# Optimization experiments

Hardware: AMD Instinct MI355X
Metric: run time of the kernel (lower is better)

## Reference

```python
import jax, jax.numpy as jnp
import numpy as np

L, N, D, C = 4, 16384, 512, 1000

def setup_inputs() -> dict:
    key = jax.random.key(0)
    k1, k2, k3, k4, k5 = jax.random.split(key, 5)
    feature = jax.random.normal(k1, (L, N, D), dtype=jnp.float32)
    mean = jax.random.normal(k2, (L, C, D), dtype=jnp.float32)
    inverse_cov = jax.random.normal(k3, (L, D, D), dtype=jnp.float32)
    weight = jax.random.uniform(k4, (L,), dtype=jnp.float32)
    top2_index = jax.random.randint(k5, (N,), 0, C, dtype=jnp.int64)
    return {"feature": feature, "mean": mean, "inverse_cov": inverse_cov,
            "weight": weight, "top2_index": top2_index}

def reference(feature, mean, inverse_cov, weight, top2_index):
    # Gather class means per sample: [L, N, D]
    final_mean = mean[:, top2_index, :]
    zero_f = feature - final_mean  # [L, N, D]
    # Diagonal of zero_f @ inv_cov @ zero_f^T without forming the NxN matrix:
    # q[l, n] = sum_{d,e} zero_f[l,n,d] * inv_cov[l,d,e] * zero_f[l,n,e]
    q = jnp.einsum('lnd,lde,lne->ln', zero_f, inverse_cov, zero_f)  # [L, N]
    return jnp.sum(weight * jnp.mean(q, axis=1))
```

## Files before the change

### kernel.cpp

```cpp
#include <hip/hip_runtime.h>
#include <hip/hip_bf16.h>
#include <stdint.h>

#define LDIM 4
#define NDIM 16384
#define DDIM 512
#define CDIM 1000
#define NSTEP 16

#define SYT_ELEMS ((size_t)LDIM * DDIM * DDIM)
#define GH_OFF   (SYT_ELEMS * 2)
#define GH_ELEMS ((size_t)LDIM * CDIM * DDIM)
#define SS_OFF   (GH_OFF + GH_ELEMS * 2)
#define SS_FLOATS ((size_t)LDIM * 1024)
#define WS_NEED  (SS_OFF + SS_FLOATS * 4)

typedef __attribute__((ext_vector_type(8))) _Float16 f16x8;
typedef __attribute__((ext_vector_type(4))) float f32x4;

__device__ __forceinline__ unsigned short f2h(float x) {
  union { _Float16 h; unsigned short u; } c; c.h = (_Float16)x; return c.u;
}
__device__ __forceinline__ float h2f(unsigned short u) {
  union { unsigned short u; _Float16 h; } c; c.u = u; return (float)c.h;
}
__device__ __forceinline__ f16x8 cvt8(float4 a, float4 b) {
  f16x8 p;
  p[0] = (_Float16)a.x; p[1] = (_Float16)a.y; p[2] = (_Float16)a.z; p[3] = (_Float16)a.w;
  p[4] = (_Float16)b.x; p[5] = (_Float16)b.y; p[6] = (_Float16)b.z; p[7] = (_Float16)b.w;
  return p;
}
__device__ __forceinline__ void gload16(const void* g, void* l) {
  __builtin_amdgcn_global_load_lds(
      (const __attribute__((address_space(1))) void*)g,
      (__attribute__((address_space(3))) void*)l, 16, 0, 0);
}

__device__ __forceinline__ size_t syt_off(int l, int d, int k) {
  return ((size_t)(l * NSTEP + (k >> 5)) * DDIM + d) * 32 +
         ((((k & 31) >> 3) + ((d >> 1) & 3)) & 3) * 8 + (k & 7);
}

#define BB0 0
#define AB0 65536
#define IDS_OFF 73728
#define SVAL_OFF 73984
#define RED_OFF 74240
#define LDS_MAIN 74272
#define LDS_PREP 65536

extern "C" __global__ void mel_mconv(const float* __restrict__ IC,
                                     unsigned short* __restrict__ SYT) {
  size_t i4 = (size_t)blockIdx.x * 256 + threadIdx.x;
  size_t base = i4 * 4;
  int l = (int)(base >> 18);
  int rem = (int)(base & 262143);
  int d = rem >> 9;
  int e = rem & 511;
  float4 v = *(const float4*)(IC + base);
  const float* icl = IC + ((size_t)l << 18);
  float t0 = icl[(size_t)(e + 0) * DDIM + d];
  float t1 = icl[(size_t)(e + 1) * DDIM + d];
  float t2 = icl[(size_t)(e + 2) * DDIM + d];
  float t3 = icl[(size_t)(e + 3) * DDIM + d];
  *(ushort4*)(SYT + syt_off(l, d, e)) =
      make_ushort4(f2h(0.5f * (v.x + t0)), f2h(0.5f * (v.y + t1)),
                   f2h(0.5f * (v.z + t2)), f2h(0.5f * (v.w + t3)));
}

extern "C" __global__ __launch_bounds__(512, 2)
void mel_prep(const float* __restrict__ MEAN, const unsigned short* __restrict__ SYT,
              unsigned short* __restrict__ GH, float* __restrict__ SS) {
  extern __shared__ __align__(16) char lds[];
  const int t = threadIdx.x, lane = t & 63, w = t >> 6;
  const int l = blockIdx.x & 3, ct = blockIdx.x >> 2;
  const int row0 = ct * 64;
  const int col0 = w * 64, lrow = lane & 15, lkg = lane >> 4;
  const int lke = lkg << 3;

  {
    const int srow = t >> 3;
    const int grow = row0 + srow;
    const float* mr = MEAN + ((size_t)l * CDIM + grow) * DDIM + ((t & 7) << 3);
    const int swb = srow * 1024 + (((t & 7) ^ (srow & 7)) << 4);
    const float4 z4 = {0.f, 0.f, 0.f, 0.f};
    for (int c = 0; c < 8; ++c) {
      float4 x = z4, y = z4;
      if (grow < CDIM) { x = *(const float4*)(mr + c * 64); y = *(const float4*)(mr + c * 64 + 4); }
      *(f16x8*)(lds + swb + c * 128) = cvt8(x, y);
    }
  }
  __syncthreads();

  f32x4 acc[4][4];
#pragma unroll
  for (int i = 0; i < 4; ++i)
#pragma unroll
    for (int j = 0; j < 4; ++j) acc[i][j] = {0.f, 0.f, 0.f, 0.f};

  for (int c = 0; c < 8; ++c) {
#pragma unroll
    for (int ks = 0; ks < 2; ++ks) {
      const int k = c * 64 + ks * 32 + lke;
      f16x8 b0 = *(const f16x8*)(SYT + syt_off(l, col0 + lrow, k));
      f16x8 b1 = *(const f16x8*)(SYT + syt_off(l, col0 + 16 + lrow, k));
      f16x8 b2 = *(const f16x8*)(SYT + syt_off(l, col0 + 32 + lrow, k));
      f16x8 b3 = *(const f16x8*)(SYT + syt_off(l, col0 + 48 + lrow, k));
      const int xo = c * 128 + ((((ks << 2) + lkg) ^ (lrow & 7)) << 4);
      f16x8 a0 = *(const f16x8*)(lds + lrow * 1024 + xo);
      f16x8 a1 = *(const f16x8*)(lds + (16 + lrow) * 1024 + xo);
      f16x8 a2 = *(const f16x8*)(lds + (32 + lrow) * 1024 + xo);
      f16x8 a3 = *(const f16x8*)(lds + (48 + lrow) * 1024 + xo);
#pragma unroll
      for (int nf = 0; nf < 4; ++nf) {
        f16x8 a = nf == 0 ? a0 : nf == 1 ? a1 : nf == 2 ? a2 : a3;
        acc[nf][0] = __builtin_amdgcn_mfma_f32_16x16x32_f16(a, b0, acc[nf][0], 0, 0, 0);
        acc[nf][1] = __builtin_amdgcn_mfma_f32_16x16x32_f16(a, b1, acc[nf][1], 0, 0, 0);
        acc[nf][2] = __builtin_amdgcn_mfma_f32_16x16x32_f16(a, b2, acc[nf][2], 0, 0, 0);
        acc[nf][3] = __builtin_amdgcn_mfma_f32_16x16x32_f16(a, b3, acc[nf][3], 0, 0, 0);
      }
    }
  }

#pragma unroll
  for (int nf = 0; nf < 4; ++nf)
#pragma unroll
    for (int r = 0; r < 4; ++r) {
      const int nloc = nf * 16 + lkg * 4 + r;
      const int grow = row0 + nloc;
      float sp = 0.f;
#pragma unroll
      for (int df = 0; df < 4; ++df) {
        const int dcol = col0 + df * 16 + lrow;
        const float av = acc[nf][df][r];
        const float mh = h2f(*(const unsigned short*)(
            lds + nloc * 1024 + (((dcol >> 3) ^ (nloc & 7)) << 4) + (dcol & 7) * 2));
        sp += mh * av;
        if (grow < CDIM) GH[((size_t)l * CDIM + grow) * DDIM + dcol] = f2h(2.f * av);
      }
      sp += __shfl_xor(sp, 1); sp += __shfl_xor(sp, 2);
      sp += __shfl_xor(sp, 4); sp += __shfl_xor(sp, 8);
      if (lrow == 0 && grow < CDIM) atomicAdd(SS + l * 1024 + grow, sp);
    }
}

extern "C" __global__ __launch_bounds__(512, 4)
void mel_main(const float* __restrict__ F, const float* __restrict__ W,
              const int* __restrict__ IDX, const unsigned short* __restrict__ SYT,
              const unsigned short* __restrict__ GH, const float* __restrict__ SS,
              float* __restrict__ OUT) {
  extern __shared__ __align__(16) char lds[];
  int* ids = (int*)(lds + IDS_OFF);
  float* sval = (float*)(lds + SVAL_OFF);
  float* red = (float*)(lds + RED_OFF);
  const int t = threadIdx.x, lane = t & 63, w = t >> 6;
  const int bid = blockIdx.x, xcd = bid & 7, l = xcd >> 1;
  const int bx = ((bid >> 3) << 1) | (xcd & 1);
  const int n0 = bx * 64;
  const int col0 = w * 64;
  const int lrow = lane & 15, lkg = lane >> 4;

  if (t < 64) {
    const int cc = IDX[n0 + t];
    ids[t] = cc;
    sval[t] = SS[l * 1024 + cc];
  }

  const int a_row = t >> 3, a_el = (t & 7) << 2;
  const float* fA = F + ((size_t)l * NDIM + n0 + a_row) * DDIM + a_el;
  const int a_wb = a_row * 64 + ((((a_el >> 3) + ((a_row >> 1) & 3)) & 3) << 4) +
                   ((a_el & 7) << 1);
  const unsigned short* syt_l = SYT + (size_t)l * NSTEP * DDIM * 32;

  {
#pragma unroll
    for (int i = 0; i < 4; ++i)
      gload16(syt_l + (size_t)(i * 512 + t) * 8,
              lds + BB0 + ((i * 512 + (t & ~63)) << 4));
    float4 x = *(const float4*)(fA);
    ushort4 h = make_ushort4(f2h(x.x), f2h(x.y), f2h(x.z), f2h(x.w));
    *(ushort4*)(lds + AB0 + a_wb) = h;
  }
  __syncthreads();

  f32x4 acc[4][4];
#pragma unroll
  for (int i = 0; i < 4; ++i)
#pragma unroll
    for (int j = 0; j < 4; ++j) acc[i][j] = {0.f, 0.f, 0.f, 0.f};

#pragma unroll 2
  for (int s = 0; s < NSTEP; ++s) {
    char* bb = lds + BB0 + (s & 1) * 32768;
    char* ab = lds + AB0 + (s & 1) * 4096;
    char* bbn = lds + BB0 + ((s + 1) & 1) * 32768;
    char* abn = lds + AB0 + ((s + 1) & 1) * 4096;
    float4 x;
    if (s < NSTEP - 1) {
      const unsigned short* src = syt_l + (size_t)(s + 1) * DDIM * 32;
#pragma unroll
      for (int i = 0; i < 4; ++i)
        gload16(src + (size_t)(i * 512 + t) * 8,
                bbn + ((i * 512 + (t & ~63)) << 4));
      x = *(const float4*)(fA + (s + 1) * 32);
    }
    f16x8 af[4], bf[4];
#pragma unroll
    for (int nf = 0; nf < 4; ++nf) {
      const int row = nf * 16 + lrow;
      af[nf] = *(const f16x8*)(ab + row * 64 + (((lkg + ((row >> 1) & 3)) & 3) << 4));
    }
#pragma unroll
    for (int df = 0; df < 4; ++df) {
      const int row = col0 + df * 16 + lrow;
      bf[df] = *(const f16x8*)(bb + row * 64 + (((lkg + ((row >> 1) & 3)) & 3) << 4));
    }
#pragma unroll
    for (int nf = 0; nf < 4; ++nf)
#pragma unroll
      for (int df = 0; df < 4; ++df)
        acc[nf][df] = __builtin_amdgcn_mfma_f32_16x16x32_f16(af[nf], bf[df], acc[nf][df], 0, 0, 0);
    if (s < NSTEP - 1) {
      ushort4 h = make_ushort4(f2h(x.x), f2h(x.y), f2h(x.z), f2h(x.w));
      *(ushort4*)(abn + a_wb) = h;
    }
    __syncthreads();
  }

  const unsigned short* gh_l = GH + (size_t)l * CDIM * DDIM;
  const float* fre = F + ((size_t)l * NDIM + n0) * DDIM;
  float tsum = 0.f;
#pragma unroll
  for (int nf = 0; nf < 4; ++nf)
#pragma unroll
    for (int df = 0; df < 4; ++df) {
      const int col = col0 + df * 16 + lrow;
      f32x4 cfrag = acc[nf][df];
#pragma unroll
      for (int r = 0; r < 4; ++r) {
        const int rowl = nf * 16 + lkg * 4 + r;
        const float fh = fre[(size_t)rowl * DDIM + col];
        const float gh = h2f(gh_l[(size_t)ids[rowl] * DDIM + col]);
        tsum += fh * (cfrag[r] - gh);
        if (w == 0 && df == 0 && lrow == 0) tsum += sval[rowl];
      }
    }
#pragma unroll
  for (int off = 32; off > 0; off >>= 1) tsum += __shfl_down(tsum, off);
  __syncthreads();
  if (lane == 0) red[w] = tsum;
  __syncthreads();
  if (t == 0) {
    float ssum = 0.f;
#pragma unroll
    for (int i = 0; i < 8; ++i) ssum += red[i];
    atomicAdd(OUT, ssum * (W[l] / (float)NDIM));
  }
}

extern "C" __global__ void mel_fallback(const float* __restrict__ F,
                                        const float* __restrict__ MEAN,
                                        const float* __restrict__ IC,
                                        const float* __restrict__ W,
                                        const int* __restrict__ IDX,
                                        float* __restrict__ OUT) {
  __shared__ float v[8][DDIM];
  __shared__ float red[256];
  const int t = threadIdx.x;
  const int l = blockIdx.y;
  const int n0 = blockIdx.x * 8;
  for (int i = t; i < 8 * DDIM; i += 256) {
    int n = i >> 9, e = i & 511;
    int c = IDX[n0 + n];
    v[n][e] = F[((size_t)l * NDIM + n0 + n) * DDIM + e] -
              MEAN[((size_t)l * CDIM + c) * DDIM + e];
  }
  __syncthreads();
  const float* icl = IC + ((size_t)l << 18);
  float part = 0.f;
  for (int rep = 0; rep < 2; ++rep) {
    int d = t + rep * 256;
    float s[8];
#pragma unroll
    for (int j = 0; j < 8; ++j) s[j] = 0.f;
    for (int e = 0; e < DDIM; ++e) {
      float m = icl[(size_t)d * DDIM + e];
#pragma unroll
      for (int j = 0; j < 8; ++j) s[j] += m * v[j][e];
    }
#pragma unroll
    for (int j = 0; j < 8; ++j) part += v[j][d] * s[j];
  }
  red[t] = part;
  __syncthreads();
  for (int o = 128; o > 0; o >>= 1) {
    if (t < o) red[t] += red[t + o];
    __syncthreads();
  }
  if (t == 0) atomicAdd(OUT, red[0] * (W[l] / (float)NDIM));
}

extern "C" void kernel_launch(void* const* d_in, const int* in_sizes, int n_in,
                              void* d_out, int out_size, void* d_ws, size_t ws_size,
                              hipStream_t stream) {
  const float* F = (const float*)d_in[0];
  const float* MEAN = (const float*)d_in[1];
  const float* IC = (const float*)d_in[2];
  const float* W = (const float*)d_in[3];
  const int* IDX = (const int*)d_in[4];
  float* OUT = (float*)d_out;

  hipMemsetAsync(d_out, 0, sizeof(float) * (size_t)out_size, stream);

  if (ws_size >= WS_NEED) {
    unsigned short* SYTp = (unsigned short*)d_ws;
    unsigned short* GHp = (unsigned short*)((char*)d_ws + GH_OFF);
    float* SSp = (float*)((char*)d_ws + SS_OFF);
    hipMemsetAsync(SSp, 0, SS_FLOATS * 4, stream);
    mel_mconv<<<dim3(1024), dim3(256), 0, stream>>>(IC, SYTp);
    (void)hipFuncSetAttribute(reinterpret_cast<const void*>(mel_prep),
                              hipFuncAttributeMaxDynamicSharedMemorySize, LDS_PREP);
    mel_prep<<<dim3(64), dim3(512), LDS_PREP, stream>>>(MEAN, SYTp, GHp, SSp);
    (void)hipFuncSetAttribute(reinterpret_cast<const void*>(mel_main),
                              hipFuncAttributeMaxDynamicSharedMemorySize, LDS_MAIN);
    mel_main<<<dim3(1024), dim3(512), LDS_MAIN, stream>>>(
        F, W, IDX, SYTp, GHp, SSp, OUT);
  } else {
    mel_fallback<<<dim3(NDIM / 8, LDIM), dim3(256), 0, stream>>>(F, MEAN, IC, W, IDX, OUT);
  }
}
```

Before: 97.26 us.

## Load B fragments directly from global, stage full A tile in LDS once

The main kernel no longer double-buffers the symmetrized inverse-covariance tile through LDS with async global-to-LDS loads. Each wave now reads its B fragments straight from global memory, which relies on L2/L1 caching since all blocks of a layer share that matrix. The whole 64x512 feature tile is converted to fp16 and written to LDS once up front, which removes the per-step __syncthreads. LDS use per block stays about the same, but the MFMA loop now waits on global load latency with no explicit prefetch, so it may stall.

Result: no change. 96.64 us (-0.6%).

```diff
diff --git a/kernel.cpp b/kernel.cpp
--- a/kernel.cpp
+++ b/kernel.cpp
@@ -30,23 +30,16 @@
   p[4] = (_Float16)b.x; p[5] = (_Float16)b.y; p[6] = (_Float16)b.z; p[7] = (_Float16)b.w;
   return p;
 }
-__device__ __forceinline__ void gload16(const void* g, void* l) {
-  __builtin_amdgcn_global_load_lds(
-      (const __attribute__((address_space(1))) void*)g,
-      (__attribute__((address_space(3))) void*)l, 16, 0, 0);
-}
 
 __device__ __forceinline__ size_t syt_off(int l, int d, int k) {
   return ((size_t)(l * NSTEP + (k >> 5)) * DDIM + d) * 32 +
          ((((k & 31) >> 3) + ((d >> 1) & 3)) & 3) * 8 + (k & 7);
 }
 
-#define BB0 0
-#define AB0 65536
-#define IDS_OFF 73728
-#define SVAL_OFF 73984
-#define RED_OFF 74240
-#define LDS_MAIN 74272
+#define IDS_OFF 65536
+#define SVAL_OFF 65792
+#define RED_OFF 66048
+#define LDS_MAIN 66080
 #define LDS_PREP 65536
 
 extern "C" __global__ void mel_mconv(const float* __restrict__ IC,
@@ -170,16 +163,15 @@
   const float* fA = F + ((size_t)l * NDIM + n0 + a_row) * DDIM + a_el;
   const int a_wb = a_row * 64 + ((((a_el >> 3) + ((a_row >> 1) & 3)) & 3) << 4) +
                    ((a_el & 7) << 1);
-  const unsigned short* syt_l = SYT + (size_t)l * NSTEP * DDIM * 32;
-
   {
-#pragma unroll
-    for (int i = 0; i < 4; ++i)
-      gload16(syt_l + (size_t)(i * 512 + t) * 8,
-              lds + BB0 + ((i * 512 + (t & ~63)) << 4));
-    float4 x = *(const float4*)(fA);
-    ushort4 h = make_ushort4(f2h(x.x), f2h(x.y), f2h(x.z), f2h(x.w));
-    *(ushort4*)(lds + AB0 + a_wb) = h;
+    float4 fv[16];
+#pragma unroll
+    for (int c = 0; c < 16; ++c) fv[c] = *(const float4*)(fA + c * 32);
+#pragma unroll
+    for (int c = 0; c < 16; ++c) {
+      ushort4 h = make_ushort4(f2h(fv[c].x), f2h(fv[c].y), f2h(fv[c].z), f2h(fv[c].w));
+      *(ushort4*)(lds + c * 4096 + a_wb) = h;
+    }
   }
   __syncthreads();
 
@@ -189,42 +181,23 @@
 #pragma unroll
     for (int j = 0; j < 4; ++j) acc[i][j] = {0.f, 0.f, 0.f, 0.f};
 
-#pragma unroll 2
+#pragma unroll 4
   for (int s = 0; s < NSTEP; ++s) {
-    char* bb = lds + BB0 + (s & 1) * 32768;
-    char* ab = lds + AB0 + (s & 1) * 4096;
-    char* bbn = lds + BB0 + ((s + 1) & 1) * 32768;
-    char* abn = lds + AB0 + ((s + 1) & 1) * 4096;
-    float4 x;
-    if (s < NSTEP - 1) {
-      const unsigned short* src = syt_l + (size_t)(s + 1) * DDIM * 32;
-#pragma unroll
-      for (int i = 0; i < 4; ++i)
-        gload16(src + (size_t)(i * 512 + t) * 8,
-                bbn + ((i * 512 + (t & ~63)) << 4));
-      x = *(const float4*)(fA + (s + 1) * 32);
-    }
-    f16x8 af[4], bf[4];
+    f16x8 bf[4], af[4];
+#pragma unroll
+    for (int df = 0; df < 4; ++df)
+      bf[df] = *(const f16x8*)(SYT + syt_off(l, col0 + df * 16 + lrow, s * 32 + lkg * 8));
 #pragma unroll
     for (int nf = 0; nf < 4; ++nf) {
       const int row = nf * 16 + lrow;
-      af[nf] = *(const f16x8*)(ab + row * 64 + (((lkg + ((row >> 1) & 3)) & 3) << 4));
-    }
-#pragma unroll
-    for (int df = 0; df < 4; ++df) {
-      const int row = col0 + df * 16 + lrow;
-      bf[df] = *(const f16x8*)(bb + row * 64 + (((lkg + ((row >> 1) & 3)) & 3) << 4));
+      af[nf] = *(const f16x8*)(lds + s * 4096 + row * 64 +
+                               (((lkg + ((row >> 1) & 3)) & 3) << 4));
     }
 #pragma unroll
     for (int nf = 0; nf < 4; ++nf)
 #pragma unroll
       for (int df = 0; df < 4; ++df)
         acc[nf][df] = __builtin_amdgcn_mfma_f32_16x16x32_f16(af[nf], bf[df], acc[nf][df], 0, 0, 0);
-    if (s < NSTEP - 1) {
-      ushort4 h = make_ushort4(f2h(x.x), f2h(x.y), f2h(x.z), f2h(x.w));
-      *(ushort4*)(abn + a_wb) = h;
-    }
-    __syncthreads();
   }
 
   const unsigned short* gh_l = GH + (size_t)l * CDIM * DDIM;
```

## Triple-buffer inverse-covariance tiles with explicit vmcnt waits in main GEMM loop

Applied to the files above, without the earlier changes.

Grows the B-tile LDS ring from two to three 32KB stages, prefetching the inverse-covariance slice two k-steps ahead via global_load_lds. It replaces __syncthreads with manual s_waitcnt vmcnt/lgkmcnt plus s_barrier so only the older loads must complete. The loop is fully unrolled, which lets the modulo-3 buffer indexing become constant. This is meant to hide more global-load latency, but it raises LDS use to about 105KB and lowers launch bounds to 2 blocks per CU, which cuts occupancy.

Result: slower. 122.5 us (+26.0%).

```diff
diff --git a/kernel.cpp b/kernel.cpp
--- a/kernel.cpp
+++ b/kernel.cpp
@@ -42,11 +42,11 @@
 }
 
 #define BB0 0
-#define AB0 65536
-#define IDS_OFF 73728
-#define SVAL_OFF 73984
-#define RED_OFF 74240
-#define LDS_MAIN 74272
+#define AB0 98304
+#define IDS_OFF 106496
+#define SVAL_OFF 106752
+#define RED_OFF 107008
+#define LDS_MAIN 107040
 #define LDS_PREP 65536
 
 extern "C" __global__ void mel_mconv(const float* __restrict__ IC,
@@ -144,7 +144,7 @@
     }
 }
 
-extern "C" __global__ __launch_bounds__(512, 4)
+extern "C" __global__ __launch_bounds__(512, 2)
 void mel_main(const float* __restrict__ F, const float* __restrict__ W,
               const int* __restrict__ IDX, const unsigned short* __restrict__ SYT,
               const unsigned short* __restrict__ GH, const float* __restrict__ SS,
@@ -173,15 +173,21 @@
   const unsigned short* syt_l = SYT + (size_t)l * NSTEP * DDIM * 32;
 
   {
+    float4 x0 = *(const float4*)(fA);
 #pragma unroll
     for (int i = 0; i < 4; ++i)
       gload16(syt_l + (size_t)(i * 512 + t) * 8,
               lds + BB0 + ((i * 512 + (t & ~63)) << 4));
-    float4 x = *(const float4*)(fA);
-    ushort4 h = make_ushort4(f2h(x.x), f2h(x.y), f2h(x.z), f2h(x.w));
-    *(ushort4*)(lds + AB0 + a_wb) = h;
-  }
-  __syncthreads();
+#pragma unroll
+    for (int i = 0; i < 4; ++i)
+      gload16(syt_l + (size_t)DDIM * 32 + (size_t)(i * 512 + t) * 8,
+              lds + BB0 + 32768 + ((i * 512 + (t & ~63)) << 4));
+    *(ushort4*)(lds + AB0 + a_wb) = make_ushort4(f2h(x0.x), f2h(x0.y), f2h(x0.z), f2h(x0.w));
+    asm volatile("s_waitcnt vmcnt(4)" ::: "memory");
+    asm volatile("s_waitcnt lgkmcnt(0)" ::: "memory");
+    __builtin_amdgcn_s_barrier();
+    __builtin_amdgcn_sched_barrier(0);
+  }
 
   f32x4 acc[4][4];
 #pragma unroll
@@ -189,20 +195,19 @@
 #pragma unroll
     for (int j = 0; j < 4; ++j) acc[i][j] = {0.f, 0.f, 0.f, 0.f};
 
-#pragma unroll 2
+#pragma unroll
   for (int s = 0; s < NSTEP; ++s) {
-    char* bb = lds + BB0 + (s & 1) * 32768;
-    char* ab = lds + AB0 + (s & 1) * 4096;
-    char* bbn = lds + BB0 + ((s + 1) & 1) * 32768;
+    const char* bb = lds + BB0 + (s % 3) * 32768;
+    const char* ab = lds + AB0 + (s & 1) * 4096;
     char* abn = lds + AB0 + ((s + 1) & 1) * 4096;
-    float4 x;
-    if (s < NSTEP - 1) {
-      const unsigned short* src = syt_l + (size_t)(s + 1) * DDIM * 32;
+    float4 xA;
+    if (s + 1 < NSTEP) xA = *(const float4*)(fA + (s + 1) * 32);
+    if (s + 2 < NSTEP) {
+      const unsigned short* src = syt_l + (size_t)(s + 2) * DDIM * 32;
+      char* bdst = lds + BB0 + ((s + 2) % 3) * 32768;
 #pragma unroll
       for (int i = 0; i < 4; ++i)
-        gload16(src + (size_t)(i * 512 + t) * 8,
-                bbn + ((i * 512 + (t & ~63)) << 4));
-      x = *(const float4*)(fA + (s + 1) * 32);
+        gload16(src + (size_t)(i * 512 + t) * 8, bdst + ((i * 512 + (t & ~63)) << 4));
     }
     f16x8 af[4], bf[4];
 #pragma unroll
@@ -212,19 +217,27 @@
     }
 #pragma unroll
     for (int df = 0; df < 4; ++df) {
-      const int row = col0 + df * 16 + lrow;
-      bf[df] = *(const f16x8*)(bb + row * 64 + (((lkg + ((row >> 1) & 3)) & 3) << 4));
+      const int dl = col0 + df * 16 + lrow;
+      bf[df] = *(const f16x8*)(bb + dl * 64 + (((lkg + ((dl >> 1) & 3)) & 3) << 4));
     }
 #pragma unroll
     for (int nf = 0; nf < 4; ++nf)
 #pragma unroll
       for (int df = 0; df < 4; ++df)
         acc[nf][df] = __builtin_amdgcn_mfma_f32_16x16x32_f16(af[nf], bf[df], acc[nf][df], 0, 0, 0);
-    if (s < NSTEP - 1) {
-      ushort4 h = make_ushort4(f2h(x.x), f2h(x.y), f2h(x.z), f2h(x.w));
-      *(ushort4*)(abn + a_wb) = h;
-    }
-    __syncthreads();
+    if (s + 1 < NSTEP) {
+      *(ushort4*)(abn + a_wb) = make_ushort4(f2h(xA.x), f2h(xA.y), f2h(xA.z), f2h(xA.w));
+    }
+    if (s + 1 < NSTEP) {
+      if (s + 2 < NSTEP) {
+        asm volatile("s_waitcnt vmcnt(4)" ::: "memory");
+      } else {
+        asm volatile("s_waitcnt vmcnt(0)" ::: "memory");
+      }
+      asm volatile("s_waitcnt lgkmcnt(0)" ::: "memory");
+      __builtin_amdgcn_s_barrier();
+      __builtin_amdgcn_sched_barrier(0);
+    }
   }
 
   const unsigned short* gh_l = GH + (size_t)l * CDIM * DDIM;
```
